# Kernel optimization log

Hardware: AMD Instinct MI355X
Metric: run time of the kernel (lower is better)

Reference implementation:

```python
import jax, jax.numpy as jnp
import numpy as np

N = 100000
E = 1600000
IN_DIM, HID, OUT = 512, 128, 16


def setup_inputs() -> dict:
    key = jax.random.key(0)
    ks = jax.random.split(key, 8)
    x = jax.random.normal(ks[0], (N, IN_DIM), dtype=jnp.float32)
    edge_index = jax.random.randint(ks[1], (2, E), 0, N, dtype=jnp.int64)
    # GCNConv params (Glorot-ish scale) and Linear head
    W1 = jax.random.normal(ks[2], (IN_DIM, HID), dtype=jnp.float32) / np.sqrt(IN_DIM)
    b1 = jnp.zeros((HID,), dtype=jnp.float32)
    W2 = jax.random.normal(ks[3], (HID, HID), dtype=jnp.float32) / np.sqrt(HID)
    b2 = jnp.zeros((HID,), dtype=jnp.float32)
    Wl = jax.random.normal(ks[4], (HID, OUT), dtype=jnp.float32) / np.sqrt(HID)
    bl = jnp.zeros((OUT,), dtype=jnp.float32)
    return {"x": x, "edge_index": edge_index, "W1": W1, "b1": b1,
            "W2": W2, "b2": b2, "Wl": Wl, "bl": bl}


def _gcn_conv(x, W, b, src, dst, deg_inv_sqrt, deg_inv):
    # h = x @ W ; out[dst] += norm * h[src]; self-loop adds h[i]/deg[i]
    h = x @ W                                           # [N, D]
    norm = deg_inv_sqrt[src] * deg_inv_sqrt[dst]        # [E]
    msgs = h[src] * norm[:, None]                       # [E, D] gather
    agg = jax.ops.segment_sum(msgs, dst, num_segments=x.shape[0])  # scatter
    agg = agg + h * deg_inv[:, None]                    # self-loop term
    return agg + b


def reference(x, edge_index, W1, b1, W2, b2, Wl, bl):
    src, dst = edge_index[0], edge_index[1]
    n = x.shape[0]
    ones = jnp.ones(src.shape[0], dtype=x.dtype)
    # degree with self-loops (PyG gcn_norm counts in-degree at target + 1)
    deg = jax.ops.segment_sum(ones, dst, num_segments=n) + 1.0
    deg_inv_sqrt = jax.lax.rsqrt(deg)
    deg_inv = 1.0 / deg

    h = _gcn_conv(x, W1, b1, src, dst, deg_inv_sqrt, deg_inv)
    h = jax.nn.relu(h)
    # dropout: inference mode (training=False) -> identity
    h = _gcn_conv(h, W2, b2, src, dst, deg_inv_sqrt, deg_inv)
    embeddings = jax.nn.relu(h)
    out = embeddings @ Wl + bl
    return out, embeddings
```

## Files before the change

### kernel.cpp

```cpp
#include <hip/hip_runtime.h>

#define NN 100000
#define EE 1600000
#define IND 512
#define HIDD 128
#define OUTD 16
#define GEMM_BLKS 1563

typedef __bf16 bf16x8 __attribute__((ext_vector_type(8)));
typedef float f32x4 __attribute__((ext_vector_type(4)));

__device__ __forceinline__ ushort f2bf(float f) {
    union { float f; uint u; } v; v.f = f;
    uint r = v.u + 0x7FFFu + ((v.u >> 16) & 1u);
    return (ushort)(r >> 16);
}

__device__ __forceinline__ uint pk2bf(float a, float b) {
    __bf16 x = (__bf16)a, y = (__bf16)b;
    ushort ux = *(ushort*)&x, uy = *(ushort*)&y;
    return (uint)ux | ((uint)uy << 16);
}

#define GLDS16(src, dst)                                              \
    __builtin_amdgcn_global_load_lds(                                 \
        (const __attribute__((address_space(1))) void*)(src),         \
        (__attribute__((address_space(3))) void*)(dst), 16, 0, 0)

__global__ void k_prep(const float* __restrict__ W1, const float* __restrict__ W2,
                       ushort* __restrict__ Wt1, ushort* __restrict__ Wt2) {
    int b = blockIdx.x, tid = threadIdx.x;
    if (b < 256) {
        int i = b * 256 + tid;
        int k = i >> 7, n = i & 127;
        Wt1[n * 512 + k] = f2bf(W1[i]);
    } else {
        int i = (b - 256) * 256 + tid;
        int k = i >> 7, n = i & 127;
        Wt2[n * 128 + k] = f2bf(W2[i]);
    }
}

__global__ void k_scan_local(const int* __restrict__ deg, int* __restrict__ incl,
                             int* __restrict__ bsum) {
    __shared__ int s[256];
    int tid = threadIdx.x;
    int i = blockIdx.x * 256 + tid;
    int v = (i < NN) ? deg[i] : 0;
    s[tid] = v;
    __syncthreads();
    for (int off = 1; off < 256; off <<= 1) {
        int t = (tid >= off) ? s[tid - off] : 0;
        __syncthreads();
        s[tid] += t;
        __syncthreads();
    }
    if (i < NN) incl[i] = s[tid];
    if (tid == 255) bsum[blockIdx.x] = s[255];
}

__global__ void k_scan_bsum(const int* __restrict__ bsum, int* __restrict__ boff, int n) {
    __shared__ int s[512];
    int tid = threadIdx.x;
    int v = (tid < n) ? bsum[tid] : 0;
    s[tid] = v;
    __syncthreads();
    for (int off = 1; off < 512; off <<= 1) {
        int t = (tid >= off) ? s[tid - off] : 0;
        __syncthreads();
        s[tid] += t;
        __syncthreads();
    }
    if (tid < n) boff[tid] = s[tid] - v;
}

__global__ void k_scan_final(const int* __restrict__ incl, const int* __restrict__ deg,
                             const int* __restrict__ boff, int* __restrict__ rs,
                             float* __restrict__ dis, float* __restrict__ dinv) {
    int i = blockIdx.x * 256 + threadIdx.x;
    if (i < NN) {
        int d = deg[i];
        int v = incl[i] + boff[i >> 8];
        rs[i] = v - d;
        if (i == NN - 1) rs[NN] = v;
        float df = (float)(d + 1);
        dis[i] = rsqrtf(df);
        dinv[i] = 1.0f / df;
    }
}

__global__ void k_fill(const int* __restrict__ src, const int* __restrict__ dst,
                       const int* __restrict__ pos, const int* __restrict__ rs,
                       const float* __restrict__ dis, int2* __restrict__ ew) {
    int i = blockIdx.x * blockDim.x + threadIdx.x;
    int stride = gridDim.x * blockDim.x;
    for (; i < EE; i += stride) {
        int d = dst[i];
        int s = src[i];
        ew[rs[d] + pos[i]] = make_int2(s, __float_as_int(dis[s] * dis[d]));
    }
}

template <int K, bool AFP32>
__device__ __forceinline__ void gemm_body(const void* __restrict__ Ap,
                                          const ushort* __restrict__ Wt,
                                          ushort* __restrict__ C, int M, int blk) {
    constexpr int NT = K / 32;
    constexpr int ABYTES = AFP32 ? 64 * 32 * 4 : 64 * 32 * 2;
    constexpr int WBYTES = 128 * 32 * 2;
    __shared__ char smem[2 * (ABYTES + WBYTES)];

    int tid = threadIdx.x;
    int row0 = blk * 64;
    int wid = tid >> 6, lane = tid & 63;
    int wm = wid * 16;
    int lm = lane & 15, lk8 = (lane >> 4) * 8;

    const float* Af = (const float*)Ap;
    const ushort* Ab16 = (const ushort*)Ap;

    f32x4 acc[8];
#pragma unroll
    for (int q = 0; q < 8; q++) acc[q] = (f32x4){0.f, 0.f, 0.f, 0.f};

    auto stage = [&](int bi, int k0) {
        char* Abase = smem + bi * ABYTES;
        char* Wbase = smem + 2 * ABYTES + bi * WBYTES;
        if (AFP32) {
#pragma unroll
            for (int j = 0; j < 2; j++) {
                int c = wid * 2 + j;
                int rp = c * 8 + (lane >> 3);
                int sl = (lane & 7) ^ (rp & 7);
                int gr2 = row0 + rp; if (gr2 >= M) gr2 = M - 1;
                GLDS16(Af + (size_t)gr2 * K + k0 + sl * 4, Abase + c * 1024);
            }
        } else {
            int c = wid;
            int rp = c * 16 + (lane >> 2);
            int sl = (lane & 3) ^ (rp & 3);
            int gr2 = row0 + rp; if (gr2 >= M) gr2 = M - 1;
            GLDS16(Ab16 + (size_t)gr2 * K + k0 + sl * 8, Abase + c * 1024);
        }
#pragma unroll
        for (int j = 0; j < 2; j++) {
            int c = wid * 2 + j;
            int rp = c * 16 + (lane >> 2);
            int sl = (lane & 3) ^ (rp & 3);
            GLDS16(Wt + (size_t)rp * K + k0 + sl * 8, Wbase + c * 1024);
        }
    };

    stage(0, 0);

    int cur = 0;
    for (int t = 0; t < NT; t++) {
        if (t + 1 < NT) {
            stage((t + 1) & 1, (t + 1) * 32);
            if (AFP32) asm volatile("s_waitcnt vmcnt(4)" ::: "memory");
            else       asm volatile("s_waitcnt vmcnt(3)" ::: "memory");
        } else {
            asm volatile("s_waitcnt vmcnt(0)" ::: "memory");
        }
        __builtin_amdgcn_s_barrier();

        char* Abase = smem + cur * ABYTES;
        char* Wbase = smem + 2 * ABYTES + cur * WBYTES;
        bf16x8 xf, wf[8];
        if (AFP32) {
            int r_ = wm + lm;
            int s0 = lk8 >> 2;
            f32x4 a0 = *(const f32x4*)(Abase + r_ * 128 + (((s0)     ^ (r_ & 7)) << 4));
            f32x4 a1 = *(const f32x4*)(Abase + r_ * 128 + (((s0 + 1) ^ (r_ & 7)) << 4));
            uint4 u;
            u.x = pk2bf(a0[0], a0[1]);
            u.y = pk2bf(a0[2], a0[3]);
            u.z = pk2bf(a1[0], a1[1]);
            u.w = pk2bf(a1[2], a1[3]);
            xf = *(bf16x8*)&u;
        } else {
            int r_ = wm + lm;
            int s = lk8 >> 3;
            uint4 u = *(const uint4*)(Abase + r_ * 64 + ((s ^ (r_ & 3)) << 4));
            xf = *(bf16x8*)&u;
        }
#pragma unroll
        for (int q = 0; q < 8; q++) {
            int n_ = q * 16 + lm;
            int s = lk8 >> 3;
            uint4 u = *(const uint4*)(Wbase + n_ * 64 + ((s ^ (n_ & 3)) << 4));
            wf[q] = *(bf16x8*)&u;
        }
#pragma unroll
        for (int q = 0; q < 8; q++)
            acc[q] = __builtin_amdgcn_mfma_f32_16x16x32_bf16(wf[q], xf, acc[q], 0, 0, 0);

        asm volatile("" ::: "memory");
        __builtin_amdgcn_s_barrier();
        cur ^= 1;
    }

    int cn4 = (lane >> 4) * 4;
    int m = row0 + wm + lm;
    if (m < M) {
#pragma unroll
        for (int q = 0; q < 8; q++) {
            int n = q * 16 + cn4;
            uint2 o;
            o.x = (uint)f2bf(acc[q][0]) | ((uint)f2bf(acc[q][1]) << 16);
            o.y = (uint)f2bf(acc[q][2]) | ((uint)f2bf(acc[q][3]) << 16);
            *(uint2*)(C + (size_t)m * 128 + n) = o;
        }
    }
}

__global__ __launch_bounds__(256, 5) void k_mega1(const float* __restrict__ x,
                                                  const ushort* __restrict__ Wt1,
                                                  ushort* __restrict__ C,
                                                  const int* __restrict__ dst,
                                                  int* __restrict__ deg,
                                                  int* __restrict__ pos) {
    int tid = threadIdx.x;
    int base = blockIdx.x * 1024;
#pragma unroll
    for (int j = 0; j < 4; j++) {
        int i = base + j * 256 + tid;
        if (i < EE) {
            int d = dst[i];
            pos[i] = atomicAdd(&deg[d], 1);
        }
    }
    gemm_body<IND, true>(x, Wt1, C, NN, blockIdx.x);
}

__global__ __launch_bounds__(256, 6) void k_gemm2(const ushort* __restrict__ A,
                                                  const ushort* __restrict__ Wt,
                                                  ushort* __restrict__ C) {
    gemm_body<HIDD, false>(A, Wt, C, NN, blockIdx.x);
}

template <bool OUTF32>
__global__ __launch_bounds__(256) void k_agg(const ushort* __restrict__ h,
                                             const int* __restrict__ rs,
                                             const int2* __restrict__ ew,
                                             const float* __restrict__ dinv,
                                             const float* __restrict__ bias,
                                             void* __restrict__ yv) {
    int node = blockIdx.x * 4 + (threadIdx.x >> 6);
    int lane = threadIdx.x & 63;
    if (node >= NN) return;
    int half = lane >> 5, c = lane & 31;
    const uint2* h64 = (const uint2*)h;

    float acc0 = 0.f, acc1 = 0.f, acc2 = 0.f, acc3 = 0.f;
    if (half == 0) {
        float dv = dinv[node];
        uint2 sv = h64[(size_t)node * 32 + c];
        acc0 = __uint_as_float(sv.x << 16) * dv;
        acc1 = __uint_as_float(sv.x & 0xffff0000u) * dv;
        acc2 = __uint_as_float(sv.y << 16) * dv;
        acc3 = __uint_as_float(sv.y & 0xffff0000u) * dv;
    }

    int e = rs[node], e1 = rs[node + 1];

#define EL(i) int2 p##i = ew[e + 2 * i + half]; \
              uint2 g##i = h64[(size_t)(uint)p##i.x * 32 + c];
#define EA(i) { float w##i = __int_as_float(p##i.y); \
    acc0 += w##i * __uint_as_float(g##i.x << 16); \
    acc1 += w##i * __uint_as_float(g##i.x & 0xffff0000u); \
    acc2 += w##i * __uint_as_float(g##i.y << 16); \
    acc3 += w##i * __uint_as_float(g##i.y & 0xffff0000u); }

    for (; e + 16 <= e1; e += 16) {
        EL(0) EL(1) EL(2) EL(3) EL(4) EL(5) EL(6) EL(7)
        EA(0) EA(1) EA(2) EA(3) EA(4) EA(5) EA(6) EA(7)
    }
    for (; e + 4 <= e1; e += 4) {
        EL(0) EL(1)
        EA(0) EA(1)
    }
    if (e + 2 <= e1) {
        EL(0)
        EA(0)
        e += 2;
    }
    if (e < e1 && half == 0) {
        int2 p = ew[e];
        uint2 g = h64[(size_t)(uint)p.x * 32 + c];
        float w = __int_as_float(p.y);
        acc0 += w * __uint_as_float(g.x << 16);
        acc1 += w * __uint_as_float(g.x & 0xffff0000u);
        acc2 += w * __uint_as_float(g.y << 16);
        acc3 += w * __uint_as_float(g.y & 0xffff0000u);
    }
#undef EL
#undef EA

    acc0 += __shfl_xor(acc0, 32, 64);
    acc1 += __shfl_xor(acc1, 32, 64);
    acc2 += __shfl_xor(acc2, 32, 64);
    acc3 += __shfl_xor(acc3, 32, 64);

    if (half == 0) {
        float4 bv = *(const float4*)(bias + c * 4);
        acc0 = fmaxf(acc0 + bv.x, 0.f);
        acc1 = fmaxf(acc1 + bv.y, 0.f);
        acc2 = fmaxf(acc2 + bv.z, 0.f);
        acc3 = fmaxf(acc3 + bv.w, 0.f);
        if (OUTF32) {
            *(float4*)((float*)yv + (size_t)node * 128 + c * 4) =
                make_float4(acc0, acc1, acc2, acc3);
        } else {
            uint2 o;
            o.x = (uint)f2bf(acc0) | ((uint)f2bf(acc1) << 16);
            o.y = (uint)f2bf(acc2) | ((uint)f2bf(acc3) << 16);
            *(uint2*)((ushort*)yv + (size_t)node * 128 + c * 4) = o;
        }
    }
}

__global__ __launch_bounds__(256) void k_out(const float* __restrict__ emb,
                                             const float* __restrict__ Wl,
                                             const float* __restrict__ bl,
                                             float* __restrict__ out) {
    __shared__ float wl_s[128 * 16];
    __shared__ float es[16][129];
    int tid = threadIdx.x;
    int row0 = blockIdx.x * 16;
#pragma unroll
    for (int p = 0; p < 8; p++) wl_s[p * 256 + tid] = Wl[p * 256 + tid];
#pragma unroll
    for (int p = 0; p < 8; p++) {
        int idx = p * 256 + tid;
        int r = idx >> 7, c = idx & 127;
        int gr = row0 + r;
        es[r][c] = (gr < NN) ? emb[(size_t)gr * 128 + c] : 0.0f;
    }
    __syncthreads();
    int r = tid >> 4, o = tid & 15;
    float acc = bl[o];
#pragma unroll
    for (int k = 0; k < 128; k++) acc += es[r][k] * wl_s[k * 16 + o];
    int gr = row0 + r;
    if (gr < NN) out[(size_t)gr * 16 + o] = acc;
}

extern "C" void kernel_launch(void* const* d_in, const int* in_sizes, int n_in,
                              void* d_out, int out_size, void* d_ws, size_t ws_size,
                              hipStream_t stream) {
    const float* x  = (const float*)d_in[0];
    const int* ei   = (const int*)d_in[1];
    const float* W1 = (const float*)d_in[2];
    const float* b1 = (const float*)d_in[3];
    const float* W2 = (const float*)d_in[4];
    const float* b2 = (const float*)d_in[5];
    const float* Wl = (const float*)d_in[6];
    const float* bl = (const float*)d_in[7];
    const int* src = ei;
    const int* dst = ei + EE;

    float* outp = (float*)d_out;
    float* emb  = outp + (size_t)NN * OUTD;

    int2* ew    = (int2*)d_ws;
    int* pos    = (int*)(ew + EE);
    ushort* h_a = (ushort*)(pos + EE);
    ushort* h_b = h_a + (size_t)NN * 128;
    ushort* Wt1 = h_b + (size_t)NN * 128;
    ushort* Wt2 = Wt1 + 128 * 512;
    int* deg    = (int*)(Wt2 + 128 * 128);
    float* dis  = (float*)(deg + NN);
    float* dinv = dis + NN;
    int* incl   = (int*)(dinv + NN);
    int* rs     = incl + NN;
    int* bsum   = rs + NN + 8;
    int* boff   = bsum + 512;

    const int NB_N = (NN + 255) / 256;

    hipMemsetAsync(deg, 0, (size_t)NN * sizeof(int), stream);
    k_prep<<<320, 256, 0, stream>>>(W1, W2, Wt1, Wt2);
    k_mega1<<<GEMM_BLKS, 256, 0, stream>>>(x, Wt1, h_a, dst, deg, pos);
    k_scan_local<<<NB_N, 256, 0, stream>>>(deg, incl, bsum);
    k_scan_bsum<<<1, 512, 0, stream>>>(bsum, boff, NB_N);
    k_scan_final<<<NB_N, 256, 0, stream>>>(incl, deg, boff, rs, dis, dinv);
    k_fill<<<2048, 256, 0, stream>>>(src, dst, pos, rs, dis, ew);

    k_agg<false><<<(NN + 3) / 4, 256, 0, stream>>>(h_a, rs, ew, dinv, b1, h_b);
    k_gemm2<<<GEMM_BLKS, 256, 0, stream>>>(h_b, Wt2, h_a);
    k_agg<true><<<(NN + 3) / 4, 256, 0, stream>>>(h_a, rs, ew, dinv, b2, emb);
    k_out<<<(NN + 15) / 16, 256, 0, stream>>>(emb, Wl, bl, outp);
}
```

Before: 370.1 us.

## Restructure GEMMs to keep weights in LDS and stream A rows via registers

The GEMM body no longer double-buffers A and W tiles through LDS with async global-to-LDS loads. Each block now loads a large slice of W (up to 256 of K) into swizzled LDS once, and each lane streams its own A row directly into registers with a four-deep prefetch. Blocks grow to 512 threads covering 128 rows, which halves the grid, and the degree-counting atomics move after the GEMM. This cuts per-step barriers and LDS traffic for A. In exchange, A loads become uncoalesced per-lane 32-byte reads, and the staged W slice uses more LDS, which may limit occupancy.

```diff
diff --git a/kernel.cpp b/kernel.cpp
--- a/kernel.cpp
+++ b/kernel.cpp
@@ -5,7 +5,7 @@
 #define IND 512
 #define HIDD 128
 #define OUTD 16
-#define GEMM_BLKS 1563
+#define GEMM_BLKS 782
 
 typedef __bf16 bf16x8 __attribute__((ext_vector_type(8)));
 typedef float f32x4 __attribute__((ext_vector_type(4)));
@@ -21,11 +21,6 @@
     ushort ux = *(ushort*)&x, uy = *(ushort*)&y;
     return (uint)ux | ((uint)uy << 16);
 }
-
-#define GLDS16(src, dst)                                              \
-    __builtin_amdgcn_global_load_lds(                                 \
-        (const __attribute__((address_space(1))) void*)(src),         \
-        (__attribute__((address_space(3))) void*)(dst), 16, 0, 0)
 
 __global__ void k_prep(const float* __restrict__ W1, const float* __restrict__ W2,
                        ushort* __restrict__ Wt1, ushort* __restrict__ Wt2) {
@@ -102,107 +97,94 @@
 }
 
 template <int K, bool AFP32>
-__device__ __forceinline__ void gemm_body(const void* __restrict__ Ap,
+__device__ __forceinline__ void gemm_ldsw(const void* __restrict__ Ap,
                                           const ushort* __restrict__ Wt,
-                                          ushort* __restrict__ C, int M, int blk) {
-    constexpr int NT = K / 32;
-    constexpr int ABYTES = AFP32 ? 64 * 32 * 4 : 64 * 32 * 2;
-    constexpr int WBYTES = 128 * 32 * 2;
-    __shared__ char smem[2 * (ABYTES + WBYTES)];
+                                          ushort* __restrict__ C, int blk) {
+    constexpr int KH = (K > 256) ? 256 : K;
+    constexpr int HALVES = K / KH;
+    constexpr int CH = KH / 8;
+    constexpr int ROWB = CH * 16;
+    constexpr int NTh = KH / 32;
+    __shared__ char Wl_s[128 * ROWB];
 
     int tid = threadIdx.x;
-    int row0 = blk * 64;
+    int row0 = blk * 128;
     int wid = tid >> 6, lane = tid & 63;
-    int wm = wid * 16;
-    int lm = lane & 15, lk8 = (lane >> 4) * 8;
-
-    const float* Af = (const float*)Ap;
-    const ushort* Ab16 = (const ushort*)Ap;
+    int lm = lane & 15, lkq = lane >> 4;
+    int m = row0 + wid * 16 + lm;
+    int mc = (m < NN) ? m : NN - 1;
+
+    const float* Arow32 = (const float*)Ap + (size_t)mc * K;
+    const ushort* Arow16 = (const ushort*)Ap + (size_t)mc * K;
 
     f32x4 acc[8];
 #pragma unroll
     for (int q = 0; q < 8; q++) acc[q] = (f32x4){0.f, 0.f, 0.f, 0.f};
 
-    auto stage = [&](int bi, int k0) {
-        char* Abase = smem + bi * ABYTES;
-        char* Wbase = smem + 2 * ABYTES + bi * WBYTES;
-        if (AFP32) {
-#pragma unroll
-            for (int j = 0; j < 2; j++) {
-                int c = wid * 2 + j;
-                int rp = c * 8 + (lane >> 3);
-                int sl = (lane & 7) ^ (rp & 7);
-                int gr2 = row0 + rp; if (gr2 >= M) gr2 = M - 1;
-                GLDS16(Af + (size_t)gr2 * K + k0 + sl * 4, Abase + c * 1024);
-            }
-        } else {
-            int c = wid;
-            int rp = c * 16 + (lane >> 2);
-            int sl = (lane & 3) ^ (rp & 3);
-            int gr2 = row0 + rp; if (gr2 >= M) gr2 = M - 1;
-            GLDS16(Ab16 + (size_t)gr2 * K + k0 + sl * 8, Abase + c * 1024);
-        }
-#pragma unroll
-        for (int j = 0; j < 2; j++) {
-            int c = wid * 2 + j;
-            int rp = c * 16 + (lane >> 2);
-            int sl = (lane & 3) ^ (rp & 3);
-            GLDS16(Wt + (size_t)rp * K + k0 + sl * 8, Wbase + c * 1024);
-        }
-    };
-
-    stage(0, 0);
-
-    int cur = 0;
-    for (int t = 0; t < NT; t++) {
-        if (t + 1 < NT) {
-            stage((t + 1) & 1, (t + 1) * 32);
-            if (AFP32) asm volatile("s_waitcnt vmcnt(4)" ::: "memory");
-            else       asm volatile("s_waitcnt vmcnt(3)" ::: "memory");
-        } else {
-            asm volatile("s_waitcnt vmcnt(0)" ::: "memory");
-        }
-        __builtin_amdgcn_s_barrier();
-
-        char* Abase = smem + cur * ABYTES;
-        char* Wbase = smem + 2 * ABYTES + cur * WBYTES;
-        bf16x8 xf, wf[8];
-        if (AFP32) {
-            int r_ = wm + lm;
-            int s0 = lk8 >> 2;
-            f32x4 a0 = *(const f32x4*)(Abase + r_ * 128 + (((s0)     ^ (r_ & 7)) << 4));
-            f32x4 a1 = *(const f32x4*)(Abase + r_ * 128 + (((s0 + 1) ^ (r_ & 7)) << 4));
-            uint4 u;
-            u.x = pk2bf(a0[0], a0[1]);
-            u.y = pk2bf(a0[2], a0[3]);
-            u.z = pk2bf(a1[0], a1[1]);
-            u.w = pk2bf(a1[2], a1[3]);
-            xf = *(bf16x8*)&u;
-        } else {
-            int r_ = wm + lm;
-            int s = lk8 >> 3;
-            uint4 u = *(const uint4*)(Abase + r_ * 64 + ((s ^ (r_ & 3)) << 4));
-            xf = *(bf16x8*)&u;
-        }
-#pragma unroll
-        for (int q = 0; q < 8; q++) {
-            int n_ = q * 16 + lm;
-            int s = lk8 >> 3;
-            uint4 u = *(const uint4*)(Wbase + n_ * 64 + ((s ^ (n_ & 3)) << 4));
-            wf[q] = *(bf16x8*)&u;
-        }
-#pragma unroll
-        for (int q = 0; q < 8; q++)
-            acc[q] = __builtin_amdgcn_mfma_f32_16x16x32_bf16(wf[q], xf, acc[q], 0, 0, 0);
-
-        asm volatile("" ::: "memory");
-        __builtin_amdgcn_s_barrier();
-        cur ^= 1;
+#pragma unroll
+    for (int h = 0; h < HALVES; h++) {
+        int kh = h * KH;
+        if (h > 0) __syncthreads();
+        {
+            int n = tid >> 2, qt = tid & 3;
+            const ushort* wsrc = Wt + (size_t)n * K + kh + qt * (KH / 4);
+#pragma unroll
+            for (int j = 0; j < CH / 4; j++) {
+                int c = qt * (CH / 4) + j;
+                uint4 v = *(const uint4*)(wsrc + j * 8);
+                int cs = c ^ (n & 7);
+                *(uint4*)(Wl_s + n * ROWB + cs * 16) = v;
+            }
+        }
+        __syncthreads();
+
+        float4 pa32[4][2];
+        uint4 pa16[4];
+#pragma unroll
+        for (int p = 0; p < 4 && p < NTh; p++) {
+            if (AFP32) {
+                const float* pp = Arow32 + kh + p * 32 + lkq * 8;
+                pa32[p][0] = *(const float4*)pp;
+                pa32[p][1] = *(const float4*)(pp + 4);
+            } else {
+                pa16[p] = *(const uint4*)(Arow16 + kh + p * 32 + lkq * 8);
+            }
+        }
+#pragma unroll
+        for (int t = 0; t < NTh; t++) {
+            constexpr int PM = 3;
+            bf16x8 xf;
+            if (AFP32) {
+                uint4 u;
+                u.x = pk2bf(pa32[t & PM][0].x, pa32[t & PM][0].y);
+                u.y = pk2bf(pa32[t & PM][0].z, pa32[t & PM][0].w);
+                u.z = pk2bf(pa32[t & PM][1].x, pa32[t & PM][1].y);
+                u.w = pk2bf(pa32[t & PM][1].z, pa32[t & PM][1].w);
+                xf = *(bf16x8*)&u;
+            } else {
+                xf = *(bf16x8*)&pa16[t & PM];
+            }
+            if (t + 4 < NTh) {
+                if (AFP32) {
+                    const float* pp = Arow32 + kh + (t + 4) * 32 + lkq * 8;
+                    pa32[t & PM][0] = *(const float4*)pp;
+                    pa32[t & PM][1] = *(const float4*)(pp + 4);
+                } else {
+                    pa16[t & PM] = *(const uint4*)(Arow16 + kh + (t + 4) * 32 + lkq * 8);
+                }
+            }
+#pragma unroll
+            for (int q = 0; q < 8; q++) {
+                int n_ = q * 16 + lm;
+                int c = t * 4 + lkq;
+                uint4 w = *(const uint4*)(Wl_s + n_ * ROWB + ((c ^ (n_ & 7)) << 4));
+                acc[q] = __builtin_amdgcn_mfma_f32_16x16x32_bf16(*(bf16x8*)&w, xf, acc[q], 0, 0, 0);
+            }
+        }
     }
 
     int cn4 = (lane >> 4) * 4;
-    int m = row0 + wm + lm;
-    if (m < M) {
+    if (m < NN) {
 #pragma unroll
         for (int q = 0; q < 8; q++) {
             int n = q * 16 + cn4;
@@ -214,29 +196,25 @@
     }
 }
 
-__global__ __launch_bounds__(256, 5) void k_mega1(const float* __restrict__ x,
+__global__ __launch_bounds__(512, 4) void k_mega1(const float* __restrict__ x,
                                                   const ushort* __restrict__ Wt1,
                                                   ushort* __restrict__ C,
                                                   const int* __restrict__ dst,
                                                   int* __restrict__ deg,
                                                   int* __restrict__ pos) {
-    int tid = threadIdx.x;
-    int base = blockIdx.x * 1024;
+    gemm_ldsw<IND, true>(x, Wt1, C, blockIdx.x);
+    int base = blockIdx.x * 2048;
 #pragma unroll
     for (int j = 0; j < 4; j++) {
-        int i = base + j * 256 + tid;
-        if (i < EE) {
-            int d = dst[i];
-            pos[i] = atomicAdd(&deg[d], 1);
-        }
-    }
-    gemm_body<IND, true>(x, Wt1, C, NN, blockIdx.x);
-}
-
-__global__ __launch_bounds__(256, 6) void k_gemm2(const ushort* __restrict__ A,
+        int i = base + j * 512 + threadIdx.x;
+        if (i < EE) pos[i] = atomicAdd(&deg[dst[i]], 1);
+    }
+}
+
+__global__ __launch_bounds__(512, 4) void k_gemm2(const ushort* __restrict__ A,
                                                   const ushort* __restrict__ Wt,
                                                   ushort* __restrict__ C) {
-    gemm_body<HIDD, false>(A, Wt, C, NN, blockIdx.x);
+    gemm_ldsw<HIDD, false>(A, Wt, C, blockIdx.x);
 }
 
 template <bool OUTF32>
@@ -381,14 +359,14 @@
 
     hipMemsetAsync(deg, 0, (size_t)NN * sizeof(int), stream);
     k_prep<<<320, 256, 0, stream>>>(W1, W2, Wt1, Wt2);
-    k_mega1<<<GEMM_BLKS, 256, 0, stream>>>(x, Wt1, h_a, dst, deg, pos);
+    k_mega1<<<GEMM_BLKS, 512, 0, stream>>>(x, Wt1, h_a, dst, deg, pos);
     k_scan_local<<<NB_N, 256, 0, stream>>>(deg, incl, bsum);
     k_scan_bsum<<<1, 512, 0, stream>>>(bsum, boff, NB_N);
     k_scan_final<<<NB_N, 256, 0, stream>>>(incl, deg, boff, rs, dis, dinv);
     k_fill<<<2048, 256, 0, stream>>>(src, dst, pos, rs, dis, ew);
 
     k_agg<false><<<(NN + 3) / 4, 256, 0, stream>>>(h_a, rs, ew, dinv, b1, h_b);
-    k_gemm2<<<GEMM_BLKS, 256, 0, stream>>>(h_b, Wt2, h_a);
+    k_gemm2<<<GEMM_BLKS, 512, 0, stream>>>(h_b, Wt2, h_a);
     k_agg<true><<<(NN + 3) / 4, 256, 0, stream>>>(h_a, rs, ew, dinv, b2, emb);
     k_out<<<(NN + 15) / 16, 256, 0, stream>>>(emb, Wl, bl, outp);
 }
```

Result: no change. 375.4 us (+1.4%).

## Restructure GEMMs to load full-K A tile into LDS and read weights from global

Applied to the files above, without the earlier changes.

Replaces the double-buffered K-loop GEMM (64-row tiles, weights staged through LDS) with a 32-row tile that loads the whole K extent of A into LDS once, then streams weight fragments straight from global/L2 into MFMAs. Each wave now covers 16 rows by 64 columns, and the grid doubles to 3125 blocks. The degree atomics are moved after the GEMM in the first kernel. This drops the per-iteration barriers and LDS weight staging, but it uses 64KB of LDS per block for fp32 A, which limits occupancy, and it re-reads the weights from cache for every block.

```diff
diff --git a/kernel.cpp b/kernel.cpp
--- a/kernel.cpp
+++ b/kernel.cpp
@@ -5,7 +5,7 @@
 #define IND 512
 #define HIDD 128
 #define OUTD 16
-#define GEMM_BLKS 1563
+#define G1_BLKS 3125
 
 typedef __bf16 bf16x8 __attribute__((ext_vector_type(8)));
 typedef float f32x4 __attribute__((ext_vector_type(4)));
@@ -102,76 +102,63 @@
 }
 
 template <int K, bool AFP32>
-__device__ __forceinline__ void gemm_body(const void* __restrict__ Ap,
-                                          const ushort* __restrict__ Wt,
-                                          ushort* __restrict__ C, int M, int blk) {
+__device__ __forceinline__ void gemm_fullk(const void* __restrict__ Ap,
+                                           const ushort* __restrict__ Wt,
+                                           ushort* __restrict__ C, int blk) {
+    constexpr int ROWB = K * (AFP32 ? 4 : 2);
     constexpr int NT = K / 32;
-    constexpr int ABYTES = AFP32 ? 64 * 32 * 4 : 64 * 32 * 2;
-    constexpr int WBYTES = 128 * 32 * 2;
-    __shared__ char smem[2 * (ABYTES + WBYTES)];
+    __shared__ char Al[32 * ROWB];
 
     int tid = threadIdx.x;
-    int row0 = blk * 64;
+    int row0 = blk * 32;
     int wid = tid >> 6, lane = tid & 63;
-    int wm = wid * 16;
-    int lm = lane & 15, lk8 = (lane >> 4) * 8;
+    int lm = lane & 15, lkq = lane >> 4;
+    int wrh = wid & 1, wn = (wid >> 1) * 64;
 
     const float* Af = (const float*)Ap;
-    const ushort* Ab16 = (const ushort*)Ap;
-
-    f32x4 acc[8];
-#pragma unroll
-    for (int q = 0; q < 8; q++) acc[q] = (f32x4){0.f, 0.f, 0.f, 0.f};
-
-    auto stage = [&](int bi, int k0) {
-        char* Abase = smem + bi * ABYTES;
-        char* Wbase = smem + 2 * ABYTES + bi * WBYTES;
-        if (AFP32) {
-#pragma unroll
-            for (int j = 0; j < 2; j++) {
-                int c = wid * 2 + j;
-                int rp = c * 8 + (lane >> 3);
-                int sl = (lane & 7) ^ (rp & 7);
-                int gr2 = row0 + rp; if (gr2 >= M) gr2 = M - 1;
-                GLDS16(Af + (size_t)gr2 * K + k0 + sl * 4, Abase + c * 1024);
-            }
-        } else {
-            int c = wid;
-            int rp = c * 16 + (lane >> 2);
-            int sl = (lane & 3) ^ (rp & 3);
-            int gr2 = row0 + rp; if (gr2 >= M) gr2 = M - 1;
-            GLDS16(Ab16 + (size_t)gr2 * K + k0 + sl * 8, Abase + c * 1024);
-        }
+    const ushort* Ab = (const ushort*)Ap;
+
+    if (AFP32) {
+#pragma unroll
+        for (int j = 0; j < 16; j++) {
+            int c = wid * 16 + j;
+            int rp = c >> 1;
+            int mc = row0 + rp; if (mc >= NN) mc = NN - 1;
+            int s = (c & 1) * 64 + lane;
+            int sg = (s & ~7) | ((s ^ rp) & 7);
+            GLDS16((const char*)(Af + (size_t)mc * K) + sg * 16, Al + c * 1024);
+        }
+    } else {
 #pragma unroll
         for (int j = 0; j < 2; j++) {
             int c = wid * 2 + j;
-            int rp = c * 16 + (lane >> 2);
-            int sl = (lane & 3) ^ (rp & 3);
-            GLDS16(Wt + (size_t)rp * K + k0 + sl * 8, Wbase + c * 1024);
-        }
-    };
-
-    stage(0, 0);
-
-    int cur = 0;
+            int rp = c * 4 + (lane >> 4);
+            int mc = row0 + rp; if (mc >= NN) mc = NN - 1;
+            int s = lane & 15;
+            int sg = s ^ (rp & 7);
+            GLDS16((const char*)(Ab + (size_t)mc * K) + sg * 16, Al + c * 1024);
+        }
+    }
+    __syncthreads();
+
+    f32x4 acc[4];
+#pragma unroll
+    for (int q = 0; q < 4; q++) acc[q] = (f32x4){0.f, 0.f, 0.f, 0.f};
+
+    int r_ = wrh * 16 + lm;
+    const char* arow = Al + r_ * ROWB;
+    int rx = r_ & 7;
+
+#pragma unroll
     for (int t = 0; t < NT; t++) {
-        if (t + 1 < NT) {
-            stage((t + 1) & 1, (t + 1) * 32);
-            if (AFP32) asm volatile("s_waitcnt vmcnt(4)" ::: "memory");
-            else       asm volatile("s_waitcnt vmcnt(3)" ::: "memory");
-        } else {
-            asm volatile("s_waitcnt vmcnt(0)" ::: "memory");
-        }
-        __builtin_amdgcn_s_barrier();
-
-        char* Abase = smem + cur * ABYTES;
-        char* Wbase = smem + 2 * ABYTES + cur * WBYTES;
-        bf16x8 xf, wf[8];
+        bf16x8 xf;
         if (AFP32) {
-            int r_ = wm + lm;
-            int s0 = lk8 >> 2;
-            f32x4 a0 = *(const f32x4*)(Abase + r_ * 128 + (((s0)     ^ (r_ & 7)) << 4));
-            f32x4 a1 = *(const f32x4*)(Abase + r_ * 128 + (((s0 + 1) ^ (r_ & 7)) << 4));
+            int s0 = t * 8 + lkq * 2;
+            int s0x = (s0 & ~7) | ((s0 ^ rx) & 7);
+            int s1 = s0 + 1;
+            int s1x = (s1 & ~7) | ((s1 ^ rx) & 7);
+            f32x4 a0 = *(const f32x4*)(arow + s0x * 16);
+            f32x4 a1 = *(const f32x4*)(arow + s1x * 16);
             uint4 u;
             u.x = pk2bf(a0[0], a0[1]);
             u.y = pk2bf(a0[2], a0[3]);
@@ -179,33 +166,25 @@
             u.w = pk2bf(a1[2], a1[3]);
             xf = *(bf16x8*)&u;
         } else {
-            int r_ = wm + lm;
-            int s = lk8 >> 3;
-            uint4 u = *(const uint4*)(Abase + r_ * 64 + ((s ^ (r_ & 3)) << 4));
+            int s = t * 4 + lkq;
+            int sx = s ^ rx;
+            uint4 u = *(const uint4*)(arow + sx * 16);
             xf = *(bf16x8*)&u;
         }
 #pragma unroll
-        for (int q = 0; q < 8; q++) {
-            int n_ = q * 16 + lm;
-            int s = lk8 >> 3;
-            uint4 u = *(const uint4*)(Wbase + n_ * 64 + ((s ^ (n_ & 3)) << 4));
-            wf[q] = *(bf16x8*)&u;
-        }
-#pragma unroll
-        for (int q = 0; q < 8; q++)
-            acc[q] = __builtin_amdgcn_mfma_f32_16x16x32_bf16(wf[q], xf, acc[q], 0, 0, 0);
-
-        asm volatile("" ::: "memory");
-        __builtin_amdgcn_s_barrier();
-        cur ^= 1;
-    }
-
-    int cn4 = (lane >> 4) * 4;
-    int m = row0 + wm + lm;
-    if (m < M) {
-#pragma unroll
-        for (int q = 0; q < 8; q++) {
-            int n = q * 16 + cn4;
+        for (int q = 0; q < 4; q++) {
+            int n_ = wn + q * 16 + lm;
+            bf16x8 wf = *(const bf16x8*)(Wt + (size_t)n_ * K + t * 32 + lkq * 8);
+            acc[q] = __builtin_amdgcn_mfma_f32_16x16x32_bf16(wf, xf, acc[q], 0, 0, 0);
+        }
+    }
+
+    int m = row0 + r_;
+    int cn4 = lkq * 4;
+    if (m < NN) {
+#pragma unroll
+        for (int q = 0; q < 4; q++) {
+            int n = wn + q * 16 + cn4;
             uint2 o;
             o.x = (uint)f2bf(acc[q][0]) | ((uint)f2bf(acc[q][1]) << 16);
             o.y = (uint)f2bf(acc[q][2]) | ((uint)f2bf(acc[q][3]) << 16);
@@ -214,29 +193,25 @@
     }
 }
 
-__global__ __launch_bounds__(256, 5) void k_mega1(const float* __restrict__ x,
+__global__ __launch_bounds__(256, 2) void k_mega1(const float* __restrict__ x,
                                                   const ushort* __restrict__ Wt1,
                                                   ushort* __restrict__ C,
                                                   const int* __restrict__ dst,
                                                   int* __restrict__ deg,
                                                   int* __restrict__ pos) {
-    int tid = threadIdx.x;
-    int base = blockIdx.x * 1024;
-#pragma unroll
-    for (int j = 0; j < 4; j++) {
-        int i = base + j * 256 + tid;
-        if (i < EE) {
-            int d = dst[i];
-            pos[i] = atomicAdd(&deg[d], 1);
-        }
-    }
-    gemm_body<IND, true>(x, Wt1, C, NN, blockIdx.x);
-}
-
-__global__ __launch_bounds__(256, 6) void k_gemm2(const ushort* __restrict__ A,
+    gemm_fullk<IND, true>(x, Wt1, C, blockIdx.x);
+    int base = blockIdx.x * 512;
+#pragma unroll
+    for (int j = 0; j < 2; j++) {
+        int i = base + j * 256 + threadIdx.x;
+        pos[i] = atomicAdd(&deg[dst[i]], 1);
+    }
+}
+
+__global__ __launch_bounds__(256, 4) void k_gemm2(const ushort* __restrict__ A,
                                                   const ushort* __restrict__ Wt,
                                                   ushort* __restrict__ C) {
-    gemm_body<HIDD, false>(A, Wt, C, NN, blockIdx.x);
+    gemm_fullk<HIDD, false>(A, Wt, C, blockIdx.x);
 }
 
 template <bool OUTF32>
@@ -381,14 +356,14 @@
 
     hipMemsetAsync(deg, 0, (size_t)NN * sizeof(int), stream);
     k_prep<<<320, 256, 0, stream>>>(W1, W2, Wt1, Wt2);
-    k_mega1<<<GEMM_BLKS, 256, 0, stream>>>(x, Wt1, h_a, dst, deg, pos);
+    k_mega1<<<G1_BLKS, 256, 0, stream>>>(x, Wt1, h_a, dst, deg, pos);
     k_scan_local<<<NB_N, 256, 0, stream>>>(deg, incl, bsum);
     k_scan_bsum<<<1, 512, 0, stream>>>(bsum, boff, NB_N);
     k_scan_final<<<NB_N, 256, 0, stream>>>(incl, deg, boff, rs, dis, dinv);
     k_fill<<<2048, 256, 0, stream>>>(src, dst, pos, rs, dis, ew);
 
     k_agg<false><<<(NN + 3) / 4, 256, 0, stream>>>(h_a, rs, ew, dinv, b1, h_b);
-    k_gemm2<<<GEMM_BLKS, 256, 0, stream>>>(h_b, Wt2, h_a);
+    k_gemm2<<<G1_BLKS, 256, 0, stream>>>(h_b, Wt2, h_a);
     k_agg<true><<<(NN + 3) / 4, 256, 0, stream>>>(h_a, rs, ew, dinv, b2, emb);
     k_out<<<(NN + 15) / 16, 256, 0, stream>>>(emb, Wl, bl, outp);
 }
```

Measured after the change: 428.1 us. 15.7% more time.

## Fuse output linear head into final aggregation and split degree-count blocks from GEMM

Applied to the files above, without the earlier changes.

The separate k_out kernel is removed. The final aggregation now computes the 128x16 linear head in registers, reducing the partial products with 32-lane xor shuffles, and writes the output rows directly. This avoids re-reading the fp32 embeddings and one launch, but adds many shuffles (16 values x 5 steps) per node in the aggregation. The degree-counting atomics are also moved from every GEMM block into 192 dedicated grid-stride blocks of the fused launch, separating atomic latency from GEMM work.

```diff
diff --git a/kernel.cpp b/kernel.cpp
--- a/kernel.cpp
+++ b/kernel.cpp
@@ -5,6 +5,7 @@
 #define IND 512
 #define HIDD 128
 #define OUTD 16
+#define DEG_BLKS 192
 #define GEMM_BLKS 1563
 
 typedef __bf16 bf16x8 __attribute__((ext_vector_type(8)));
@@ -220,17 +221,13 @@
                                                   const int* __restrict__ dst,
                                                   int* __restrict__ deg,
                                                   int* __restrict__ pos) {
-    int tid = threadIdx.x;
-    int base = blockIdx.x * 1024;
-#pragma unroll
-    for (int j = 0; j < 4; j++) {
-        int i = base + j * 256 + tid;
-        if (i < EE) {
-            int d = dst[i];
-            pos[i] = atomicAdd(&deg[d], 1);
-        }
-    }
-    gemm_body<IND, true>(x, Wt1, C, NN, blockIdx.x);
+    if (blockIdx.x < DEG_BLKS) {
+        int i = blockIdx.x * 256 + threadIdx.x;
+        int stride = DEG_BLKS * 256;
+        for (; i < EE; i += stride) pos[i] = atomicAdd(&deg[dst[i]], 1);
+    } else {
+        gemm_body<IND, true>(x, Wt1, C, NN, blockIdx.x - DEG_BLKS);
+    }
 }
 
 __global__ __launch_bounds__(256, 6) void k_gemm2(const ushort* __restrict__ A,
@@ -239,13 +236,16 @@
     gemm_body<HIDD, false>(A, Wt, C, NN, blockIdx.x);
 }
 
-template <bool OUTF32>
+template <int MODE>
 __global__ __launch_bounds__(256) void k_agg(const ushort* __restrict__ h,
                                              const int* __restrict__ rs,
                                              const int2* __restrict__ ew,
                                              const float* __restrict__ dinv,
                                              const float* __restrict__ bias,
-                                             void* __restrict__ yv) {
+                                             void* __restrict__ yv,
+                                             const float* __restrict__ Wl,
+                                             const float* __restrict__ bl,
+                                             float* __restrict__ outp) {
     int node = blockIdx.x * 4 + (threadIdx.x >> 6);
     int lane = threadIdx.x & 63;
     if (node >= NN) return;
@@ -308,42 +308,47 @@
         acc1 = fmaxf(acc1 + bv.y, 0.f);
         acc2 = fmaxf(acc2 + bv.z, 0.f);
         acc3 = fmaxf(acc3 + bv.w, 0.f);
-        if (OUTF32) {
-            *(float4*)((float*)yv + (size_t)node * 128 + c * 4) =
-                make_float4(acc0, acc1, acc2, acc3);
-        } else {
+        if (MODE == 0) {
             uint2 o;
             o.x = (uint)f2bf(acc0) | ((uint)f2bf(acc1) << 16);
             o.y = (uint)f2bf(acc2) | ((uint)f2bf(acc3) << 16);
             *(uint2*)((ushort*)yv + (size_t)node * 128 + c * 4) = o;
-        }
-    }
-}
-
-__global__ __launch_bounds__(256) void k_out(const float* __restrict__ emb,
-                                             const float* __restrict__ Wl,
-                                             const float* __restrict__ bl,
-                                             float* __restrict__ out) {
-    __shared__ float wl_s[128 * 16];
-    __shared__ float es[16][129];
-    int tid = threadIdx.x;
-    int row0 = blockIdx.x * 16;
-#pragma unroll
-    for (int p = 0; p < 8; p++) wl_s[p * 256 + tid] = Wl[p * 256 + tid];
-#pragma unroll
-    for (int p = 0; p < 8; p++) {
-        int idx = p * 256 + tid;
-        int r = idx >> 7, c = idx & 127;
-        int gr = row0 + r;
-        es[r][c] = (gr < NN) ? emb[(size_t)gr * 128 + c] : 0.0f;
-    }
-    __syncthreads();
-    int r = tid >> 4, o = tid & 15;
-    float acc = bl[o];
-#pragma unroll
-    for (int k = 0; k < 128; k++) acc += es[r][k] * wl_s[k * 16 + o];
-    int gr = row0 + r;
-    if (gr < NN) out[(size_t)gr * 16 + o] = acc;
+        } else {
+            *(float4*)((float*)yv + (size_t)node * 128 + c * 4) =
+                make_float4(acc0, acc1, acc2, acc3);
+            float part[16];
+            {
+                const float4* w0 = (const float4*)(Wl + (c * 4 + 0) * 16);
+                const float4* w1 = (const float4*)(Wl + (c * 4 + 1) * 16);
+                const float4* w2 = (const float4*)(Wl + (c * 4 + 2) * 16);
+                const float4* w3 = (const float4*)(Wl + (c * 4 + 3) * 16);
+#pragma unroll
+                for (int g4 = 0; g4 < 4; g4++) {
+                    float4 a = w0[g4], b = w1[g4], cc = w2[g4], d = w3[g4];
+                    part[g4 * 4 + 0] = acc0 * a.x + acc1 * b.x + acc2 * cc.x + acc3 * d.x;
+                    part[g4 * 4 + 1] = acc0 * a.y + acc1 * b.y + acc2 * cc.y + acc3 * d.y;
+                    part[g4 * 4 + 2] = acc0 * a.z + acc1 * b.z + acc2 * cc.z + acc3 * d.z;
+                    part[g4 * 4 + 3] = acc0 * a.w + acc1 * b.w + acc2 * cc.w + acc3 * d.w;
+                }
+            }
+#pragma unroll
+            for (int s = 1; s < 32; s <<= 1) {
+#pragma unroll
+                for (int o = 0; o < 16; o++) part[o] += __shfl_xor(part[o], s, 64);
+            }
+            if (c == 0) {
+                float* op = outp + (size_t)node * 16;
+#pragma unroll
+                for (int g4 = 0; g4 < 4; g4++) {
+                    float4 bv4 = *(const float4*)(bl + g4 * 4);
+                    *(float4*)(op + g4 * 4) = make_float4(part[g4 * 4 + 0] + bv4.x,
+                                                          part[g4 * 4 + 1] + bv4.y,
+                                                          part[g4 * 4 + 2] + bv4.z,
+                                                          part[g4 * 4 + 3] + bv4.w);
+                }
+            }
+        }
+    }
 }
 
 extern "C" void kernel_launch(void* const* d_in, const int* in_sizes, int n_in,
@@ -381,14 +386,15 @@
 
     hipMemsetAsync(deg, 0, (size_t)NN * sizeof(int), stream);
     k_prep<<<320, 256, 0, stream>>>(W1, W2, Wt1, Wt2);
-    k_mega1<<<GEMM_BLKS, 256, 0, stream>>>(x, Wt1, h_a, dst, deg, pos);
+    k_mega1<<<DEG_BLKS + GEMM_BLKS, 256, 0, stream>>>(x, Wt1, h_a, dst, deg, pos);
     k_scan_local<<<NB_N, 256, 0, stream>>>(deg, incl, bsum);
     k_scan_bsum<<<1, 512, 0, stream>>>(bsum, boff, NB_N);
     k_scan_final<<<NB_N, 256, 0, stream>>>(incl, deg, boff, rs, dis, dinv);
     k_fill<<<2048, 256, 0, stream>>>(src, dst, pos, rs, dis, ew);
 
-    k_agg<false><<<(NN + 3) / 4, 256, 0, stream>>>(h_a, rs, ew, dinv, b1, h_b);
+    k_agg<0><<<(NN + 3) / 4, 256, 0, stream>>>(h_a, rs, ew, dinv, b1, h_b,
+                                               nullptr, nullptr, nullptr);
     k_gemm2<<<GEMM_BLKS, 256, 0, stream>>>(h_b, Wt2, h_a);
-    k_agg<true><<<(NN + 3) / 4, 256, 0, stream>>>(h_a, rs, ew, dinv, b2, emb);
-    k_out<<<(NN + 15) / 16, 256, 0, stream>>>(emb, Wl, bl, outp);
-}
+    k_agg<1><<<(NN + 3) / 4, 256, 0, stream>>>(h_a, rs, ew, dinv, b2, emb,
+                                               Wl, bl, outp);
+}
```

Result: slower. 413.8 us (+11.8%).
